# Performance work log

Measured on AMD Instinct MI355X. Metric: run time of the kernel, lower is better.

Reference implementation:

```python
import jax, jax.numpy as jnp
import numpy as np

N, E, F, C, ED, G, D = 50000, 1000000, 30, 64, 11, 1024, 256


def setup_inputs() -> dict:
    key = jax.random.key(0)
    ks = jax.random.split(key, 20)
    rn = lambda k, shape, s=0.1: jax.random.normal(k, shape, jnp.float32) * s
    return {
        "x": rn(ks[0], (N, F), 1.0),
        "edge_attr": jax.random.uniform(ks[1], (E, ED), jnp.float32),
        "W0": rn(ks[2], (F, C)), "asrc0": rn(ks[3], (C,)), "adst0": rn(ks[4], (C,)),
        "We0": rn(ks[5], (ED, C)), "ae0": rn(ks[6], (C,)), "Wres0": rn(ks[7], (F, C)),
        "b0": jnp.zeros((C,), jnp.float32),
        "W": rn(ks[8], (3, C, C)), "asrc": rn(ks[9], (3, C)), "adst": rn(ks[10], (3, C)),
        "We": rn(ks[11], (3, ED, C)), "ae": rn(ks[12], (3, C)), "Wres": rn(ks[13], (3, C, C)),
        "b": jnp.zeros((3, C), jnp.float32),
        "Wout": rn(ks[14], (2 * C, D)), "bout": jnp.zeros((D,), jnp.float32),
        "edge_index": jax.random.randint(ks[15], (2, E), 0, N),
        "batch_index": jnp.sort(jax.random.randint(ks[16], (N,), 0, G)),
    }


def _gat(x, src, dst, edge_attr, W, asrc, adst, We, ae, Wres, b):
    """PyG GATConv (heads=1) with edge_dim and residual=True."""
    n = x.shape[0]
    h = x @ W                                   # [N, C]
    e = edge_attr @ We                          # [E, C]
    alpha = (jnp.sum(h * asrc, -1)[src]
             + jnp.sum(h * adst, -1)[dst]
             + jnp.sum(e * ae, -1))             # [E]
    alpha = jax.nn.leaky_relu(alpha, 0.2)
    m = jax.ops.segment_max(alpha, dst, num_segments=n)
    a = jnp.exp(alpha - m[dst])
    s = jax.ops.segment_sum(a, dst, num_segments=n)
    a = a / (s[dst] + 1e-16)                    # per-dst softmax
    out = jax.ops.segment_sum(a[:, None] * h[src], dst, num_segments=n)
    return out + x @ Wres + b


def reference(x, edge_attr, W0, asrc0, adst0, We0, ae0, Wres0, b0,
              W, asrc, adst, We, ae, Wres, b, Wout, bout,
              edge_index, batch_index):
    src, dst = edge_index[0], edge_index[1]
    h = jax.nn.leaky_relu(
        _gat(x, src, dst, edge_attr, W0, asrc0, adst0, We0, ae0, Wres0, b0), 0.01)
    for i in range(3):  # conv1..conv3 (fixed small layer loop)
        h = _gat(h, src, dst, edge_attr, W[i], asrc[i], adst[i],
                 We[i], ae[i], Wres[i], b[i])
        if i < 2:
            h = jax.nn.leaky_relu(h, 0.01)
    gmax = jax.ops.segment_max(h, batch_index, num_segments=G)
    gmax = jnp.where(jnp.isfinite(gmax), gmax, 0.0)  # empty graphs -> 0
    cnt = jax.ops.segment_sum(jnp.ones((h.shape[0],), h.dtype), batch_index,
                              num_segments=G)
    gmean = jax.ops.segment_sum(h, batch_index, num_segments=G) / jnp.maximum(cnt, 1.0)[:, None]
    pooled = jax.nn.leaky_relu(jnp.concatenate([gmax, gmean], axis=1), 0.01)
    return pooled @ Wout + bout
```

## Files before the change

kernel.cpp:

```cpp
#include <hip/hip_runtime.h>
#include <hip/hip_fp16.h>

#define NN 50000
#define NE 1000000
#define FIN0 30
#define C 64
#define ED 11
#define NG 1024
#define DOUT 256
#define NBIN 196
#define PA_EDGES 1024

typedef unsigned long long ull;

__global__ __launch_bounds__(256) void hist196_kernel(const int* __restrict__ dst,
    int* __restrict__ bcnt){
  __shared__ int h[256];
  int t=threadIdx.x;
  h[t]=0;
  __syncthreads();
  for(int i=blockIdx.x*256+t;i<NE;i+=gridDim.x*256)
    atomicAdd(&h[dst[i]>>8],1);
  __syncthreads();
  if(h[t]) atomicAdd(&bcnt[t],h[t]);
}

__global__ __launch_bounds__(256) void scan196_kernel(const int* __restrict__ bcnt,
    int* __restrict__ bbase, int* __restrict__ gcur){
  __shared__ int p[256];
  int t=threadIdx.x;
  int v=bcnt[t];
  p[t]=v; __syncthreads();
  #pragma unroll
  for(int off=1;off<256;off<<=1){
    int u=(t>=off)?p[t-off]:0;
    __syncthreads(); p[t]+=u; __syncthreads();
  }
  int ex=p[t]-v;
  if(t<=NBIN) bbase[t]=ex;
  if(t<NBIN)  gcur[t]=ex;
}

__global__ __launch_bounds__(256) void grow_kernel(const int* __restrict__ batch,
    int* __restrict__ growptr){
  int i=blockIdx.x*256+threadIdx.x;
  if(i>=NN) return;
  int bi=batch[i];
  int bp=(i==0)?-1:batch[i-1];
  for(int g=bp+1;g<=bi;++g) growptr[g]=i;
  if(i==NN-1){ for(int g=bi+1;g<=NG;++g) growptr[g]=NN; }
}

__global__ __launch_bounds__(256) void part_kernel(const int* __restrict__ dst,
    const int* __restrict__ src, const float* __restrict__ edge_attr,
    const float* __restrict__ We0, const float* __restrict__ ae0,
    const float* __restrict__ We,  const float* __restrict__ ae,
    int* __restrict__ gcur, uint4* __restrict__ prec){
  __shared__ uint4 lrec[PA_EDGES];
  __shared__ float sw[4][ED];
  __shared__ int hist[256], sc[256], lofs[256], bb[256];
  __shared__ int wsum[4];
  int t=threadIdx.x;
  hist[t]=0;
  if(t<4*ED){
    int l=t/ED, j=t%ED;
    const float* wp=(l==0)? (We0+(size_t)j*C) : (We+((size_t)(l-1)*ED+j)*C);
    const float* ap=(l==0)? ae0 : (ae+(size_t)(l-1)*C);
    float s=0.f;
    for(int c=0;c<C;++c) s+=wp[c]*ap[c];
    sw[l][j]=s;
  }
  __syncthreads();
  size_t e0=(size_t)blockIdx.x*PA_EDGES;
  int cnt=(int)min((size_t)PA_EDGES,(size_t)NE-e0);
  int dreg[4], sreg[4];
  #pragma unroll
  for(int r=0;r<4;++r){
    int i=r*256+t;
    if(i<cnt){
      dreg[r]=dst[e0+i]; sreg[r]=src[e0+i];
      atomicAdd(&hist[dreg[r]>>8],1);
    } else dreg[r]=-1;
  }
  __syncthreads();
  int v=hist[t];
  int inc=v;
  #pragma unroll
  for(int off=1;off<64;off<<=1){
    int u=__shfl_up(inc,off,64);
    if((t&63)>=off) inc+=u;
  }
  if((t&63)==63) wsum[t>>6]=inc;
  __syncthreads();
  int woff=0;
  int myw=t>>6;
  #pragma unroll
  for(int k=0;k<3;++k) if(k<myw) woff+=wsum[k];
  int ex=woff+inc-v;
  sc[t]=ex;
  lofs[t]=ex;
  bb[t]=(v>0)?atomicAdd(&gcur[t],v):0;
  __syncthreads();
  #pragma unroll
  for(int r=0;r<4;++r){
    int i=r*256+t;
    if(i<cnt){
      const float* ea=edge_attr+(e0+i)*(size_t)ED;
      float d0=0,d1=0,d2=0,d3=0;
      #pragma unroll
      for(int j=0;j<ED;++j){
        float ev=ea[j];
        d0=fmaf(ev,sw[0][j],d0);
        d1=fmaf(ev,sw[1][j],d1);
        d2=fmaf(ev,sw[2][j],d2);
        d3=fmaf(ev,sw[3][j],d3);
      }
      uint4 rec;
      rec.x=(unsigned)dreg[r]; rec.y=(unsigned)sreg[r];
      rec.z=(unsigned)__half_as_ushort(__float2half(d0))
           |((unsigned)__half_as_ushort(__float2half(d1))<<16);
      rec.w=(unsigned)__half_as_ushort(__float2half(d2))
           |((unsigned)__half_as_ushort(__float2half(d3))<<16);
      int slot=atomicAdd(&lofs[dreg[r]>>8],1);
      lrec[slot]=rec;
    }
  }
  __syncthreads();
  for(int i=t;i<cnt;i+=256){
    uint4 rec=lrec[i];
    int b=(int)(rec.x>>8);
    int g=bb[b]+i-sc[b];
    prec[g]=rec;
  }
}

__global__ __launch_bounds__(256) void build_kernel(const uint4* __restrict__ prec,
    const int* __restrict__ bbase,
    int* __restrict__ rowptr, int* __restrict__ src_csr, ushort* __restrict__ edch){
  __shared__ int cnt[256], cur[256];
  __shared__ int wsum[4];
  int t=threadIdx.x, b=blockIdx.x;
  int n0=b<<8;
  cnt[t]=0;
  __syncthreads();
  int beg=bbase[b], endd=bbase[b+1];
  for(int j=beg+t;j<endd;j+=256)
    atomicAdd(&cnt[(int)prec[j].x-n0],1);
  __syncthreads();
  int v=cnt[t];
  int inc=v;
  #pragma unroll
  for(int off=1;off<64;off<<=1){
    int u=__shfl_up(inc,off,64);
    if((t&63)>=off) inc+=u;
  }
  if((t&63)==63) wsum[t>>6]=inc;
  __syncthreads();
  int woff=0;
  int myw=t>>6;
  #pragma unroll
  for(int k=0;k<3;++k) if(k<myw) woff+=wsum[k];
  int ex=woff+inc-v;
  cur[t]=beg+ex;
  if(n0+t<NN) rowptr[n0+t]=beg+ex;
  if(b==0&&t==0) rowptr[NN]=NE;
  __syncthreads();
  for(int j=beg+t;j<endd;j+=256){
    uint4 r=prec[j];
    int d=(int)r.x, s=(int)r.y;
    int pos=atomicAdd(&cur[d-n0],1);
    src_csr[pos]=s;
    edch[pos]                =(ushort)(r.z&0xffffu);
    edch[(size_t)NE+pos]     =(ushort)(r.z>>16);
    edch[2*(size_t)NE+pos]   =(ushort)(r.w&0xffffu);
    edch[3*(size_t)NE+pos]   =(ushort)(r.w>>16);
  }
}

template<int FIN, int SXS>
__global__ __launch_bounds__(256) void feat_kernel(const float* __restrict__ in,
    const float* __restrict__ W, const float* __restrict__ Wres,
    const float* __restrict__ bvec, const float* __restrict__ av_src,
    const float* __restrict__ av_dst,
    __half* __restrict__ hW16, float* __restrict__ outb,
    float* __restrict__ as_, float* __restrict__ ad_){
  __shared__ float sW[FIN*C], sR[FIN*C];
  __shared__ float sx[64*SXS];
  __shared__ float sb[C], ss[C], sd[C];
  int tid=threadIdx.x;
  if(tid<C){ sb[tid]=bvec[tid]; ss[tid]=av_src[tid]; sd[tid]=av_dst[tid]; }
  for(int i=tid;i<FIN*C;i+=256){ sW[i]=W[i]; sR[i]=Wres[i]; }
  int nbase=blockIdx.x*64;
  int nvalid=min(64,NN-nbase);
  if constexpr (FIN==64){
    const float4* in4=(const float4*)(in+(size_t)nbase*64);
    for(int i=tid;i<1024;i+=256){
      int n=i>>4, k=(i&15)*4;
      float4 v=(n<nvalid)?in4[i]:make_float4(0.f,0.f,0.f,0.f);
      *(float4*)&sx[n*SXS+k]=v;
    }
  } else {
    for(int i=tid;i<64*FIN;i+=256){
      int n=i/FIN, k=i-n*FIN;
      sx[n*SXS+k]=(n<nvalid)?in[(size_t)(nbase+n)*FIN+k]:0.f;
    }
  }
  __syncthreads();
  int w=tid>>6, lane=tid&63;
  int ng=lane>>4, cl=lane&15;
  int n0=w*16+ng*4;
  int c0=cl*4;
  float hw[4][4]={}, hr[4][4]={};
  const float* sxp=&sx[n0*SXS];
  #pragma unroll 2
  for(int k=0;k<FIN;k+=2){
    float4 wv0=*(const float4*)&sW[k*C+c0];
    float4 rv0=*(const float4*)&sR[k*C+c0];
    float4 wv1=*(const float4*)&sW[(k+1)*C+c0];
    float4 rv1=*(const float4*)&sR[(k+1)*C+c0];
    float2 x0=*(const float2*)&sxp[k];
    float2 x1=*(const float2*)&sxp[SXS+k];
    float2 x2=*(const float2*)&sxp[2*SXS+k];
    float2 x3=*(const float2*)&sxp[3*SXS+k];
    float xa[4]={x0.x,x1.x,x2.x,x3.x};
    float xb[4]={x0.y,x1.y,x2.y,x3.y};
    #pragma unroll
    for(int r=0;r<4;++r){
      hw[r][0]=fmaf(xa[r],wv0.x,hw[r][0]);
      hw[r][1]=fmaf(xa[r],wv0.y,hw[r][1]);
      hw[r][2]=fmaf(xa[r],wv0.z,hw[r][2]);
      hw[r][3]=fmaf(xa[r],wv0.w,hw[r][3]);
      hr[r][0]=fmaf(xa[r],rv0.x,hr[r][0]);
      hr[r][1]=fmaf(xa[r],rv0.y,hr[r][1]);
      hr[r][2]=fmaf(xa[r],rv0.z,hr[r][2]);
      hr[r][3]=fmaf(xa[r],rv0.w,hr[r][3]);
      hw[r][0]=fmaf(xb[r],wv1.x,hw[r][0]);
      hw[r][1]=fmaf(xb[r],wv1.y,hw[r][1]);
      hw[r][2]=fmaf(xb[r],wv1.z,hw[r][2]);
      hw[r][3]=fmaf(xb[r],wv1.w,hw[r][3]);
      hr[r][0]=fmaf(xb[r],rv1.x,hr[r][0]);
      hr[r][1]=fmaf(xb[r],rv1.y,hr[r][1]);
      hr[r][2]=fmaf(xb[r],rv1.z,hr[r][2]);
      hr[r][3]=fmaf(xb[r],rv1.w,hr[r][3]);
    }
  }
  float s0=ss[c0], s1=ss[c0+1], s2=ss[c0+2], s3=ss[c0+3];
  float d0=sd[c0], d1=sd[c0+1], d2=sd[c0+2], d3=sd[c0+3];
  float b0v=sb[c0], b1v=sb[c0+1], b2v=sb[c0+2], b3v=sb[c0+3];
  #pragma unroll
  for(int r=0;r<4;++r){
    int n=n0+r;
    float ps=hw[r][0]*s0+hw[r][1]*s1+hw[r][2]*s2+hw[r][3]*s3;
    float pd=hw[r][0]*d0+hw[r][1]*d1+hw[r][2]*d2+hw[r][3]*d3;
    #pragma unroll
    for(int off=1;off<16;off<<=1){ ps+=__shfl_xor(ps,off,64); pd+=__shfl_xor(pd,off,64); }
    if(n<nvalid){
      size_t gn=(size_t)(nbase+n);
      ushort4 hv;
      hv.x=__half_as_ushort(__float2half(hw[r][0]));
      hv.y=__half_as_ushort(__float2half(hw[r][1]));
      hv.z=__half_as_ushort(__float2half(hw[r][2]));
      hv.w=__half_as_ushort(__float2half(hw[r][3]));
      *(ushort4*)&hW16[gn*C+c0]=hv;
      float4 ov;
      ov.x=hr[r][0]+b0v; ov.y=hr[r][1]+b1v; ov.z=hr[r][2]+b2v; ov.w=hr[r][3]+b3v;
      *(float4*)&outb[gn*C+c0]=ov;
      if(cl==0){ as_[gn]=ps; ad_[gn]=pd; }
    }
  }
}

__device__ __forceinline__ void acc8(float* a, float at, uint4 u){
  __half2 h0=*(__half2*)&u.x, h1=*(__half2*)&u.y, h2=*(__half2*)&u.z, h3=*(__half2*)&u.w;
  float2 f0=__half22float2(h0), f1=__half22float2(h1);
  float2 f2=__half22float2(h2), f3=__half22float2(h3);
  a[0]=fmaf(at,f0.x,a[0]); a[1]=fmaf(at,f0.y,a[1]);
  a[2]=fmaf(at,f1.x,a[2]); a[3]=fmaf(at,f1.y,a[3]);
  a[4]=fmaf(at,f2.x,a[4]); a[5]=fmaf(at,f2.y,a[5]);
  a[6]=fmaf(at,f3.x,a[6]); a[7]=fmaf(at,f3.y,a[7]);
}

__global__ __launch_bounds__(256) void agg_kernel(const int* __restrict__ rowptr,
    const int* __restrict__ src_csr, const ushort* __restrict__ edc_l,
    const float* __restrict__ as_, const float* __restrict__ ad_,
    const __half* __restrict__ hW16, float* __restrict__ outb, int relu){
  __shared__ float2 sws[4][64];
  int w=threadIdx.x>>6, lane=threadIdx.x&63;
  int half=lane>>5, hl=lane&31;
  int n0=blockIdx.x*8+w*2;
  int nidx=n0+half;
  int beg=rowptr[nidx], end=rowptr[nidx+1];
  int deg=end-beg;
  const uint4* hw4=(const uint4*)hW16;

  if(__all(deg<=32)){
    float ad_n=ad_[nidx];
    int j=beg+hl;
    float al=-INFINITY; int sl=0;
    if(hl<deg){
      sl=src_csr[j];
      float a=as_[sl]+ad_n+__half2float(__ushort_as_half(edc_l[j]));
      al=(a>0.f)?a:0.2f*a;
    }
    float mn=al;
    #pragma unroll
    for(int off=16;off;off>>=1) mn=fmaxf(mn,__shfl_xor(mn,off,64));
    float wl=(hl<deg)?__expf(al-mn):0.f;
    float s=wl;
    #pragma unroll
    for(int off=16;off;off>>=1) s+=__shfl_xor(s,off,64);
    float2 pr; pr.x=wl; pr.y=__int_as_float(sl);
    sws[w][lane]=pr;
    int g=hl>>3, gl=hl&7;
    float acc[8]={0.f,0.f,0.f,0.f,0.f,0.f,0.f,0.f};
    int base=half*32;
    int t=g;
    for(; t+4<deg; t+=8){
      float2 r0=sws[w][base+t], r1=sws[w][base+t+4];
      uint4 u0=hw4[(size_t)__float_as_int(r0.y)*8+gl];
      uint4 u1=hw4[(size_t)__float_as_int(r1.y)*8+gl];
      acc8(acc,r0.x,u0);
      acc8(acc,r1.x,u1);
    }
    if(t<deg){
      float2 r=sws[w][base+t];
      uint4 u=hw4[(size_t)__float_as_int(r.y)*8+gl];
      acc8(acc,r.x,u);
    }
    #pragma unroll
    for(int off=8;off<=16;off<<=1){
      #pragma unroll
      for(int i=0;i<8;++i) acc[i]+=__shfl_xor(acc[i],off,64);
    }
    if(hl<8){
      float denom=s+1e-16f;
      size_t o0=(size_t)nidx*C+hl*8;
      float4 oa=*(float4*)&outb[o0];
      float4 ob=*(float4*)&outb[o0+4];
      float4 va,vb;
      va.x=acc[0]/denom+oa.x; va.y=acc[1]/denom+oa.y;
      va.z=acc[2]/denom+oa.z; va.w=acc[3]/denom+oa.w;
      vb.x=acc[4]/denom+ob.x; vb.y=acc[5]/denom+ob.y;
      vb.z=acc[6]/denom+ob.z; vb.w=acc[7]/denom+ob.w;
      if(relu){
        va.x=(va.x>0.f)?va.x:0.01f*va.x; va.y=(va.y>0.f)?va.y:0.01f*va.y;
        va.z=(va.z>0.f)?va.z:0.01f*va.z; va.w=(va.w>0.f)?va.w:0.01f*va.w;
        vb.x=(vb.x>0.f)?vb.x:0.01f*vb.x; vb.y=(vb.y>0.f)?vb.y:0.01f*vb.y;
        vb.z=(vb.z>0.f)?vb.z:0.01f*vb.z; vb.w=(vb.w>0.f)?vb.w:0.01f*vb.w;
      }
      *(float4*)&outb[o0]=va;
      *(float4*)&outb[o0+4]=vb;
    }
    return;
  }

  for(int h=0;h<2;++h){
    int m=n0+h;
    int bh=__shfl(beg,h*32,64);
    int dh=__shfl(deg,h*32,64);
    float ad_n=ad_[m];
    int g2=lane>>3, gl2=lane&7;
    float s=0.f;
    float acc[8]={0.f,0.f,0.f,0.f,0.f,0.f,0.f,0.f};
    if(dh<=64){
      int j=bh+lane;
      float al=-INFINITY; int sl=0;
      if(lane<dh){
        sl=src_csr[j];
        float a=as_[sl]+ad_n+__half2float(__ushort_as_half(edc_l[j]));
        al=(a>0.f)?a:0.2f*a;
      }
      float mn=al;
      #pragma unroll
      for(int off=32;off;off>>=1) mn=fmaxf(mn,__shfl_xor(mn,off,64));
      float wl=(lane<dh)?__expf(al-mn):0.f;
      s=wl;
      #pragma unroll
      for(int off=32;off;off>>=1) s+=__shfl_xor(s,off,64);
      float2 pr; pr.x=wl; pr.y=__int_as_float(sl);
      sws[w][lane]=pr;
      int t=g2;
      for(; t+8<dh; t+=16){
        float2 r0=sws[w][t], r1=sws[w][t+8];
        uint4 u0=hw4[(size_t)__float_as_int(r0.y)*8+gl2];
        uint4 u1=hw4[(size_t)__float_as_int(r1.y)*8+gl2];
        acc8(acc,r0.x,u0);
        acc8(acc,r1.x,u1);
      }
      if(t<dh){
        float2 r=sws[w][t];
        uint4 u=hw4[(size_t)__float_as_int(r.y)*8+gl2];
        acc8(acc,r.x,u);
      }
    } else {
      float m_=-INFINITY;
      for(int base=bh;base<bh+dh;base+=64){
        int j=base+lane;
        float al=-INFINITY; int sl=0;
        if(j<bh+dh){
          sl=src_csr[j];
          float a=as_[sl]+ad_n+__half2float(__ushort_as_half(edc_l[j]));
          al=(a>0.f)?a:0.2f*a;
        }
        float cm=al;
        #pragma unroll
        for(int off=32;off;off>>=1) cm=fmaxf(cm,__shfl_xor(cm,off,64));
        float mn=fmaxf(m_,cm);
        float scale=(m_==-INFINITY)?0.f:__expf(m_-mn);
        s*=scale;
        #pragma unroll
        for(int i=0;i<8;++i) acc[i]*=scale;
        float wl=(j<bh+dh)?__expf(al-mn):0.f;
        float cs=wl;
        #pragma unroll
        for(int off=32;off;off>>=1) cs+=__shfl_xor(cs,off,64);
        s+=cs; m_=mn;
        float2 pr; pr.x=wl; pr.y=__int_as_float(sl);
        sws[w][lane]=pr;
        int cnt=min(64,bh+dh-base);
        int t=g2;
        for(; t+8<cnt; t+=16){
          float2 r0=sws[w][t], r1=sws[w][t+8];
          uint4 u0=hw4[(size_t)__float_as_int(r0.y)*8+gl2];
          uint4 u1=hw4[(size_t)__float_as_int(r1.y)*8+gl2];
          acc8(acc,r0.x,u0);
          acc8(acc,r1.x,u1);
        }
        if(t<cnt){
          float2 r=sws[w][t];
          uint4 u=hw4[(size_t)__float_as_int(r.y)*8+gl2];
          acc8(acc,r.x,u);
        }
      }
    }
    #pragma unroll
    for(int off=8;off<64;off<<=1){
      #pragma unroll
      for(int i=0;i<8;++i) acc[i]+=__shfl_xor(acc[i],off,64);
    }
    if(g2==0){
      float denom=s+1e-16f;
      size_t o0=(size_t)m*C+gl2*8;
      float4 oa=*(float4*)&outb[o0];
      float4 ob=*(float4*)&outb[o0+4];
      float4 va,vb;
      va.x=acc[0]/denom+oa.x; va.y=acc[1]/denom+oa.y;
      va.z=acc[2]/denom+oa.z; va.w=acc[3]/denom+oa.w;
      vb.x=acc[4]/denom+ob.x; vb.y=acc[5]/denom+ob.y;
      vb.z=acc[6]/denom+ob.z; vb.w=acc[7]/denom+ob.w;
      if(relu){
        va.x=(va.x>0.f)?va.x:0.01f*va.x; va.y=(va.y>0.f)?va.y:0.01f*va.y;
        va.z=(va.z>0.f)?va.z:0.01f*va.z; va.w=(va.w>0.f)?va.w:0.01f*va.w;
        vb.x=(vb.x>0.f)?vb.x:0.01f*vb.x; vb.y=(vb.y>0.f)?vb.y:0.01f*vb.y;
        vb.z=(vb.z>0.f)?vb.z:0.01f*vb.z; vb.w=(vb.w>0.f)?vb.w:0.01f*vb.w;
      }
      *(float4*)&outb[o0]=va;
      *(float4*)&outb[o0+4]=vb;
    }
  }
}

__global__ __launch_bounds__(256) void pool_kernel(const float* __restrict__ h,
    const int* __restrict__ growptr, float* __restrict__ pooled){
  int w=threadIdx.x>>6, lane=threadIdx.x&63;
  int g=blockIdx.x*4+w;
  if(g>=NG) return;
  int beg=growptr[g], end=growptr[g+1];
  float mx=-INFINITY, sm=0.f;
  for(int n=beg;n<end;++n){ float v=h[(size_t)n*C+lane]; mx=fmaxf(mx,v); sm+=v; }
  int cnt=end-beg;
  float gm=(cnt==0)?0.f:mx;
  float mean=sm/fmaxf((float)cnt,1.f);
  gm=(gm>0.f)?gm:0.01f*gm;
  mean=(mean>0.f)?mean:0.01f*mean;
  pooled[(size_t)g*128+lane]=gm;
  pooled[(size_t)g*128+64+lane]=mean;
}

__global__ __launch_bounds__(256) void out_kernel(const float* __restrict__ pooled,
    const float* __restrict__ Wout, const float* __restrict__ bout,
    float* __restrict__ out){
  __shared__ float sp[128];
  int g=blockIdx.x, d=threadIdx.x;
  if(d<128) sp[d]=pooled[(size_t)g*128+d];
  __syncthreads();
  float o=bout[d];
  for(int k=0;k<128;++k) o=fmaf(sp[k],Wout[k*DOUT+d],o);
  out[(size_t)g*DOUT+d]=o;
}

extern "C" void kernel_launch(void* const* d_in, const int* in_sizes, int n_in,
                              void* d_out, int out_size, void* d_ws, size_t ws_size,
                              hipStream_t stream){
  const float* x        =(const float*)d_in[0];
  const float* edge_attr=(const float*)d_in[1];
  const float* W0       =(const float*)d_in[2];
  const float* asrc0    =(const float*)d_in[3];
  const float* adst0    =(const float*)d_in[4];
  const float* We0      =(const float*)d_in[5];
  const float* ae0      =(const float*)d_in[6];
  const float* Wres0    =(const float*)d_in[7];
  const float* b0       =(const float*)d_in[8];
  const float* W        =(const float*)d_in[9];
  const float* asrc     =(const float*)d_in[10];
  const float* adst     =(const float*)d_in[11];
  const float* We       =(const float*)d_in[12];
  const float* ae       =(const float*)d_in[13];
  const float* Wres     =(const float*)d_in[14];
  const float* b        =(const float*)d_in[15];
  const float* Wout     =(const float*)d_in[16];
  const float* bout     =(const float*)d_in[17];
  const int* edge_index =(const int*)d_in[18];
  const int* batch_index=(const int*)d_in[19];
  const int* src=edge_index;
  const int* dst=edge_index+NE;

  char* p=(char*)d_ws;
  auto take=[&](size_t bytes)->void*{ void* r=(void*)p; p+=(bytes+255)&~(size_t)255; return r; };
  int* rowptr  =(int*)take((size_t)(NN+1)*4);
  int* growptr =(int*)take((size_t)(NG+1)*4);
  int* bcnt    =(int*)take((size_t)256*4);
  int* bbase   =(int*)take((size_t)256*4);
  int* gcur    =(int*)take((size_t)256*4);
  int* src_csr =(int*)take((size_t)NE*4);
  float* as_   =(float*)take((size_t)NN*4);
  float* ad_   =(float*)take((size_t)NN*4);
  ushort* edch =(ushort*)take((size_t)NE*4*2);
  __half* hW16 =(__half*)take((size_t)NN*C*2);
  float* bufA  =(float*)take((size_t)NN*C*4);
  uint4* prec  =(uint4*)take((size_t)NE*16);
  float* bufB  =(float*)prec;
  float* pooled=(float*)take((size_t)NG*128*4);
  (void)ws_size; (void)in_sizes; (void)n_in; (void)out_size;

  hipMemsetAsync(bcnt,0,(size_t)256*4,stream);
  hist196_kernel<<<1024,256,0,stream>>>(dst,bcnt);
  scan196_kernel<<<1,256,0,stream>>>(bcnt,bbase,gcur);
  grow_kernel<<<(NN+255)/256,256,0,stream>>>(batch_index,growptr);

  part_kernel<<<(NE+PA_EDGES-1)/PA_EDGES,256,0,stream>>>(dst,src,edge_attr,
      We0,ae0,We,ae,gcur,prec);
  build_kernel<<<NBIN,256,0,stream>>>(prec,bbase,rowptr,src_csr,edch);

  const int nblkF=(NN+63)/64;
  const int nblkA=NN/8;
  feat_kernel<FIN0,36><<<nblkF,256,0,stream>>>(x,W0,Wres0,b0,asrc0,adst0,hW16,bufA,as_,ad_);
  agg_kernel<<<nblkA,256,0,stream>>>(rowptr,src_csr,edch,as_,ad_,hW16,bufA,1);
  float* bin=bufA; float* bo=bufB;
  for(int i=0;i<3;++i){
    feat_kernel<C,68><<<nblkF,256,0,stream>>>(bin,W+(size_t)i*C*C,Wres+(size_t)i*C*C,
        b+(size_t)i*C,asrc+(size_t)i*C,adst+(size_t)i*C,hW16,bo,as_,ad_);
    agg_kernel<<<nblkA,256,0,stream>>>(rowptr,src_csr,edch+(size_t)(i+1)*NE,as_,ad_,hW16,bo,(i<2)?1:0);
    float* t=bin; bin=bo; bo=t;
  }
  pool_kernel<<<(NG+3)/4,256,0,stream>>>(bin,growptr,pooled);
  out_kernel<<<NG,256,0,stream>>>(pooled,Wout,bout,(float*)d_out);
}
```

Baseline: 307.6 us.

## Fuse hist/grow and pool/out kernels; restructure low-degree aggregation gather

Merges the histogram and graph-row-pointer kernels into one launch and fuses pooling with the output projection, which removes two launches and the intermediate pooled buffer. The low-degree aggregation path now pre-normalizes the softmax weights and splits the 64 channels into two passes. Each pass has 4 lanes per row and 8 edge groups, which raises edge-level parallelism per gather and drops the per-output divides. In exchange, the fused pool kernel runs only 64 threads per graph in the reduction phase, and the aggregation makes two passes over the source indices.

```diff
diff --git a/kernel.cpp b/kernel.cpp
--- a/kernel.cpp
+++ b/kernel.cpp
@@ -13,16 +13,25 @@
 
 typedef unsigned long long ull;
 
-__global__ __launch_bounds__(256) void hist196_kernel(const int* __restrict__ dst,
-    int* __restrict__ bcnt){
-  __shared__ int h[256];
+__global__ __launch_bounds__(256) void histgrow_kernel(const int* __restrict__ dst,
+    int* __restrict__ bcnt, const int* __restrict__ batch, int* __restrict__ growptr){
   int t=threadIdx.x;
-  h[t]=0;
-  __syncthreads();
-  for(int i=blockIdx.x*256+t;i<NE;i+=gridDim.x*256)
-    atomicAdd(&h[dst[i]>>8],1);
-  __syncthreads();
-  if(h[t]) atomicAdd(&bcnt[t],h[t]);
+  if(blockIdx.x<1024){
+    __shared__ int h[256];
+    h[t]=0;
+    __syncthreads();
+    for(int i=blockIdx.x*256+t;i<NE;i+=1024*256)
+      atomicAdd(&h[dst[i]>>8],1);
+    __syncthreads();
+    if(h[t]) atomicAdd(&bcnt[t],h[t]);
+  } else {
+    int i=(int)(blockIdx.x-1024)*256+t;
+    if(i>=NN) return;
+    int bi=batch[i];
+    int bp=(i==0)?-1:batch[i-1];
+    for(int g=bp+1;g<=bi;++g) growptr[g]=i;
+    if(i==NN-1){ for(int g=bi+1;g<=NG;++g) growptr[g]=NN; }
+  }
 }
 
 __global__ __launch_bounds__(256) void scan196_kernel(const int* __restrict__ bcnt,
@@ -39,16 +48,6 @@
   int ex=p[t]-v;
   if(t<=NBIN) bbase[t]=ex;
   if(t<NBIN)  gcur[t]=ex;
-}
-
-__global__ __launch_bounds__(256) void grow_kernel(const int* __restrict__ batch,
-    int* __restrict__ growptr){
-  int i=blockIdx.x*256+threadIdx.x;
-  if(i>=NN) return;
-  int bi=batch[i];
-  int bp=(i==0)?-1:batch[i-1];
-  for(int g=bp+1;g<=bi;++g) growptr[g]=i;
-  if(i==NN-1){ for(int g=bi+1;g<=NG;++g) growptr[g]=NN; }
 }
 
 __global__ __launch_bounds__(256) void part_kernel(const int* __restrict__ dst,
@@ -309,47 +308,48 @@
     float s=wl;
     #pragma unroll
     for(int off=16;off;off>>=1) s+=__shfl_xor(s,off,64);
-    float2 pr; pr.x=wl; pr.y=__int_as_float(sl);
+    float2 pr; pr.x=wl/(s+1e-16f); pr.y=__int_as_float(sl);
     sws[w][lane]=pr;
-    int g=hl>>3, gl=hl&7;
-    float acc[8]={0.f,0.f,0.f,0.f,0.f,0.f,0.f,0.f};
+    int g=hl>>2, gl=hl&3;
     int base=half*32;
-    int t=g;
-    for(; t+4<deg; t+=8){
-      float2 r0=sws[w][base+t], r1=sws[w][base+t+4];
-      uint4 u0=hw4[(size_t)__float_as_int(r0.y)*8+gl];
-      uint4 u1=hw4[(size_t)__float_as_int(r1.y)*8+gl];
-      acc8(acc,r0.x,u0);
-      acc8(acc,r1.x,u1);
-    }
-    if(t<deg){
-      float2 r=sws[w][base+t];
-      uint4 u=hw4[(size_t)__float_as_int(r.y)*8+gl];
-      acc8(acc,r.x,u);
-    }
     #pragma unroll
-    for(int off=8;off<=16;off<<=1){
+    for(int pass=0;pass<2;++pass){
+      float acc[8]={0.f,0.f,0.f,0.f,0.f,0.f,0.f,0.f};
+      size_t rowoff=(size_t)(pass*4+gl);
+      int t=g;
+      for(; t+8<deg; t+=16){
+        float2 r0=sws[w][base+t], r1=sws[w][base+t+8];
+        uint4 u0=hw4[(size_t)__float_as_int(r0.y)*8+rowoff];
+        uint4 u1=hw4[(size_t)__float_as_int(r1.y)*8+rowoff];
+        acc8(acc,r0.x,u0);
+        acc8(acc,r1.x,u1);
+      }
+      if(t<deg){
+        float2 r=sws[w][base+t];
+        uint4 u=hw4[(size_t)__float_as_int(r.y)*8+rowoff];
+        acc8(acc,r.x,u);
+      }
       #pragma unroll
-      for(int i=0;i<8;++i) acc[i]+=__shfl_xor(acc[i],off,64);
-    }
-    if(hl<8){
-      float denom=s+1e-16f;
-      size_t o0=(size_t)nidx*C+hl*8;
-      float4 oa=*(float4*)&outb[o0];
-      float4 ob=*(float4*)&outb[o0+4];
-      float4 va,vb;
-      va.x=acc[0]/denom+oa.x; va.y=acc[1]/denom+oa.y;
-      va.z=acc[2]/denom+oa.z; va.w=acc[3]/denom+oa.w;
-      vb.x=acc[4]/denom+ob.x; vb.y=acc[5]/denom+ob.y;
-      vb.z=acc[6]/denom+ob.z; vb.w=acc[7]/denom+ob.w;
-      if(relu){
-        va.x=(va.x>0.f)?va.x:0.01f*va.x; va.y=(va.y>0.f)?va.y:0.01f*va.y;
-        va.z=(va.z>0.f)?va.z:0.01f*va.z; va.w=(va.w>0.f)?va.w:0.01f*va.w;
-        vb.x=(vb.x>0.f)?vb.x:0.01f*vb.x; vb.y=(vb.y>0.f)?vb.y:0.01f*vb.y;
-        vb.z=(vb.z>0.f)?vb.z:0.01f*vb.z; vb.w=(vb.w>0.f)?vb.w:0.01f*vb.w;
-      }
-      *(float4*)&outb[o0]=va;
-      *(float4*)&outb[o0+4]=vb;
+      for(int off=4;off<=16;off<<=1){
+        #pragma unroll
+        for(int i=0;i<8;++i) acc[i]+=__shfl_xor(acc[i],off,64);
+      }
+      if(hl<4){
+        size_t o0=(size_t)nidx*C+pass*32+hl*8;
+        float4 oa=*(float4*)&outb[o0];
+        float4 ob=*(float4*)&outb[o0+4];
+        float4 va,vb;
+        va.x=acc[0]+oa.x; va.y=acc[1]+oa.y; va.z=acc[2]+oa.z; va.w=acc[3]+oa.w;
+        vb.x=acc[4]+ob.x; vb.y=acc[5]+ob.y; vb.z=acc[6]+ob.z; vb.w=acc[7]+ob.w;
+        if(relu){
+          va.x=(va.x>0.f)?va.x:0.01f*va.x; va.y=(va.y>0.f)?va.y:0.01f*va.y;
+          va.z=(va.z>0.f)?va.z:0.01f*va.z; va.w=(va.w>0.f)?va.w:0.01f*va.w;
+          vb.x=(vb.x>0.f)?vb.x:0.01f*vb.x; vb.y=(vb.y>0.f)?vb.y:0.01f*vb.y;
+          vb.z=(vb.z>0.f)?vb.z:0.01f*vb.z; vb.w=(vb.w>0.f)?vb.w:0.01f*vb.w;
+        }
+        *(float4*)&outb[o0]=va;
+        *(float4*)&outb[o0+4]=vb;
+      }
     }
     return;
   }
@@ -460,33 +460,26 @@
   }
 }
 
-__global__ __launch_bounds__(256) void pool_kernel(const float* __restrict__ h,
-    const int* __restrict__ growptr, float* __restrict__ pooled){
-  int w=threadIdx.x>>6, lane=threadIdx.x&63;
-  int g=blockIdx.x*4+w;
-  if(g>=NG) return;
+__global__ __launch_bounds__(256) void poolout_kernel(const float* __restrict__ h,
+    const int* __restrict__ growptr, const float* __restrict__ Wout,
+    const float* __restrict__ bout, float* __restrict__ out){
+  __shared__ float sp[128];
+  int t=threadIdx.x, g=blockIdx.x;
   int beg=growptr[g], end=growptr[g+1];
-  float mx=-INFINITY, sm=0.f;
-  for(int n=beg;n<end;++n){ float v=h[(size_t)n*C+lane]; mx=fmaxf(mx,v); sm+=v; }
-  int cnt=end-beg;
-  float gm=(cnt==0)?0.f:mx;
-  float mean=sm/fmaxf((float)cnt,1.f);
-  gm=(gm>0.f)?gm:0.01f*gm;
-  mean=(mean>0.f)?mean:0.01f*mean;
-  pooled[(size_t)g*128+lane]=gm;
-  pooled[(size_t)g*128+64+lane]=mean;
-}
-
-__global__ __launch_bounds__(256) void out_kernel(const float* __restrict__ pooled,
-    const float* __restrict__ Wout, const float* __restrict__ bout,
-    float* __restrict__ out){
-  __shared__ float sp[128];
-  int g=blockIdx.x, d=threadIdx.x;
-  if(d<128) sp[d]=pooled[(size_t)g*128+d];
-  __syncthreads();
-  float o=bout[d];
-  for(int k=0;k<128;++k) o=fmaf(sp[k],Wout[k*DOUT+d],o);
-  out[(size_t)g*DOUT+d]=o;
+  if(t<64){
+    float mx=-INFINITY, sm=0.f;
+    for(int n=beg;n<end;++n){ float v=h[(size_t)n*C+t]; mx=fmaxf(mx,v); sm+=v; }
+    int cnt=end-beg;
+    float gm=(cnt==0)?0.f:mx;
+    float mean=sm/fmaxf((float)cnt,1.f);
+    gm=(gm>0.f)?gm:0.01f*gm;
+    mean=(mean>0.f)?mean:0.01f*mean;
+    sp[t]=gm; sp[64+t]=mean;
+  }
+  __syncthreads();
+  float o=bout[t];
+  for(int k=0;k<128;++k) o=fmaf(sp[k],Wout[k*DOUT+t],o);
+  out[(size_t)g*DOUT+t]=o;
 }
 
 extern "C" void kernel_launch(void* const* d_in, const int* in_sizes, int n_in,
@@ -530,13 +523,11 @@
   float* bufA  =(float*)take((size_t)NN*C*4);
   uint4* prec  =(uint4*)take((size_t)NE*16);
   float* bufB  =(float*)prec;
-  float* pooled=(float*)take((size_t)NG*128*4);
   (void)ws_size; (void)in_sizes; (void)n_in; (void)out_size;
 
   hipMemsetAsync(bcnt,0,(size_t)256*4,stream);
-  hist196_kernel<<<1024,256,0,stream>>>(dst,bcnt);
+  histgrow_kernel<<<1024+(NN+255)/256,256,0,stream>>>(dst,bcnt,batch_index,growptr);
   scan196_kernel<<<1,256,0,stream>>>(bcnt,bbase,gcur);
-  grow_kernel<<<(NN+255)/256,256,0,stream>>>(batch_index,growptr);
 
   part_kernel<<<(NE+PA_EDGES-1)/PA_EDGES,256,0,stream>>>(dst,src,edge_attr,
       We0,ae0,We,ae,gcur,prec);
@@ -553,6 +544,5 @@
     agg_kernel<<<nblkA,256,0,stream>>>(rowptr,src_csr,edch+(size_t)(i+1)*NE,as_,ad_,hW16,bo,(i<2)?1:0);
     float* t=bin; bin=bo; bo=t;
   }
-  pool_kernel<<<(NG+3)/4,256,0,stream>>>(bin,growptr,pooled);
-  out_kernel<<<NG,256,0,stream>>>(pooled,Wout,bout,(float*)d_out);
-}
+  poolout_kernel<<<NG,256,0,stream>>>(bin,growptr,Wout,bout,(float*)d_out);
+}
```

Result: slower. 320.4 us (+4.2%).
